# Optimization experiments

Measured on AMD Instinct MI355X. Metric: run time of the kernel, lower is better.

The kernel has to match this reference:

```python
import jax, jax.numpy as jnp
import numpy as np

K = 16

def _knn_idx(pts, k):
    # pts: [B, 3, N] -> idx [B, N, k] (self-inclusive nearest neighbors)
    inner = -2.0 * jnp.einsum('bdn,bdm->bnm', pts, pts)
    xx = jnp.sum(pts * pts, axis=1)  # [B, N]
    pd = -xx[:, :, None] - inner - xx[:, None, :]  # negative squared distance
    _, idx = jax.lax.top_k(pd, k)
    return idx

def _gather(feats, idx):
    # feats: [B, N, D], idx: [B, N, k] -> [B, N, k, D]
    return jax.vmap(lambda f, i: f[i])(feats, idx)

def _conv1x1(x, w, b):
    # x: [B, Cin, N], w: [Cout, Cin], b: [Cout]
    return jnp.einsum('oi,bin->bon', w, x) + b[None, :, None]

def _linear(x, w, b):
    # x: [B, N, Din], w: [Dout, Din]
    return jnp.einsum('bnd,od->bno', x, w) + b

def _local_cov(pts, idx):
    # pts: [B, 3, N] -> [B, 12, N]
    nb = _gather(jnp.swapaxes(pts, 1, 2), idx)  # [B, N, k, 3]
    outer = nb[:, :, 0, :, None] * nb[:, :, 1, None, :]  # [B, N, 3, 3]
    B, N = pts.shape[0], pts.shape[2]
    outer = jnp.swapaxes(outer.reshape(B, N, 9), 1, 2)  # [B, 9, N]
    return jnp.concatenate([pts, outer], axis=1)

def _local_maxpool(x, idx):
    # x: [B, D, N] -> [B, N, D]
    nb = _gather(jnp.swapaxes(x, 1, 2), idx)  # [B, N, k, D]
    return jnp.max(nb, axis=2)

def setup_inputs() -> dict:
    key = jax.random.key(0)
    ks = jax.random.split(key, 20)
    def w(k, shape):
        return jax.random.normal(k, shape, dtype=jnp.float32) * 0.05
    pts = jax.random.normal(ks[0], (8, 3, 4096), dtype=jnp.float32)
    return {
        'pts': pts,
        'm1w1': w(ks[1], (64, 12)), 'm1b1': w(ks[2], (64,)),
        'm1w2': w(ks[3], (64, 64)), 'm1b2': w(ks[4], (64,)),
        'm1w3': w(ks[5], (64, 64)), 'm1b3': w(ks[6], (64,)),
        'l1w': w(ks[7], (64, 64)), 'l1b': w(ks[8], (64,)),
        'c1w': w(ks[9], (128, 64)), 'c1b': w(ks[10], (128,)),
        'l2w': w(ks[11], (128, 128)), 'l2b': w(ks[12], (128,)),
        'c2w': w(ks[13], (1024, 128)), 'c2b': w(ks[14], (1024,)),
        'm2w1': w(ks[15], (512, 1024)), 'm2b1': w(ks[16], (512,)),
        'm2w2': w(ks[17], (512, 512)), 'm2b2': w(ks[18], (512,)),
    }

def reference(pts, m1w1, m1b1, m1w2, m1b2, m1w3, m1b3, l1w, l1b,
              c1w, c1b, l2w, l2b, c2w, c2b, m2w1, m2b1, m2w2, m2b2):
    idx = _knn_idx(pts, K)  # [B, N, k]
    x = _local_cov(pts, idx)  # [B, 12, N]
    # mlp1: three 1x1 convs with ReLU
    x = jax.nn.relu(_conv1x1(x, m1w1, m1b1))
    x = jax.nn.relu(_conv1x1(x, m1w2, m1b2))
    x = jax.nn.relu(_conv1x1(x, m1w3, m1b3))  # [B, 64, N]
    # graph layer
    x = _local_maxpool(x, idx)          # [B, N, 64]
    x = _linear(x, l1w, l1b)            # [B, N, 64]
    x = jnp.swapaxes(x, 1, 2)           # [B, 64, N]
    x = jax.nn.relu(_conv1x1(x, c1w, c1b))  # [B, 128, N]
    x = _local_maxpool(x, idx)          # [B, N, 128]
    x = _linear(x, l2w, l2b)            # [B, N, 128]
    x = jnp.swapaxes(x, 1, 2)           # [B, 128, N]
    x = _conv1x1(x, c2w, c2b)           # [B, 1024, N]
    # global max pool
    x = jnp.max(x, axis=2, keepdims=True)  # [B, 1024, 1]
    # mlp2
    x = jax.nn.relu(_conv1x1(x, m2w1, m2b1))
    x = _conv1x1(x, m2w2, m2b2)  # [B, 512, 1]
    return x.reshape(-1, 512)
```

## Files before the change

### kernel.cpp

```cpp
#include <hip/hip_runtime.h>
#include <cfloat>

#define NBATCH 8
#define NPTS   4096
#define KNN    16
#define PPB    32
#define NSL    8
#define CAP    24

typedef unsigned short u16;
typedef __attribute__((ext_vector_type(8))) short short8;
typedef __attribute__((ext_vector_type(4))) float f32x4;

__device__ __forceinline__ float relu_f(float x) { return x > 0.f ? x : 0.f; }

__device__ __forceinline__ void bf16_split(float v, u16& hi, u16& lo)
{
    unsigned u = __float_as_uint(v);
    unsigned hb = (u + 0x7FFFu + ((u >> 16) & 1u)) >> 16;
    float hf = __uint_as_float(hb << 16);
    float l = v - hf;
    unsigned ul = __float_as_uint(l);
    unsigned lb = (ul + 0x7FFFu + ((ul >> 16) & 1u)) >> 16;
    hi = (u16)hb; lo = (u16)lb;
}

__global__ __launch_bounds__(256)
void knn_kernel(const float* __restrict__ pts, int* __restrict__ idxout)
{
    __shared__ __align__(16) float4 tile[NSL * 129];
    __shared__ float  kl[PPB * NSL * 8];
    __shared__ float  thr[PPB];
    __shared__ int    cnt[PPB];

    const int b = blockIdx.y, tid = threadIdx.x;
    const int ptl = tid >> 3, r = tid & 7;
    const int n = blockIdx.x * PPB + ptl;
    const float* pb = pts + (size_t)b * 3 * NPTS;

    const float sx = pb[n], sy = pb[NPTS + n], sz = pb[2 * NPTS + n];

    float k8[8];
#pragma unroll
    for (int s = 0; s < 8; ++s) k8[s] = -FLT_MAX;

    const float4* slice = tile + r * 129;

    for (int t = 0; t < 4; ++t) {
        if (t) __syncthreads();
        for (int i = tid; i < 1024; i += 256) {
            int j = t * 1024 + i;
            float x = pb[j], y = pb[NPTS + j], z = pb[2 * NPTS + j];
            float xx = __fadd_rn(__fadd_rn(__fmul_rn(x, x), __fmul_rn(y, y)),
                                 __fmul_rn(z, z));
            tile[(i >> 7) * 129 + (i & 127)] = make_float4(x, y, z, xx);
        }
        __syncthreads();
#pragma unroll 8
        for (int ii = 0; ii < 128; ++ii) {
            float4 c = slice[ii];
            float dt = __fmaf_rn(sx, c.x, __fmaf_rn(sy, c.y, __fmul_rn(sz, c.z)));
            float pd = __fmaf_rn(2.f, dt, -c.w);
            float old0 = k8[0];
#pragma unroll
            for (int s = 7; s >= 1; --s)
                k8[s] = __builtin_amdgcn_fmed3f(k8[s - 1], k8[s], pd);
            k8[0] = fmaxf(old0, pd);
        }
    }

#pragma unroll
    for (int s = 0; s < 8; ++s) kl[(ptl * NSL + r) * 8 + s] = k8[s];
    __syncthreads();

    if (r == 0) {
        const float* L = kl + ptl * 64;
        int p0 = 0, p1 = 0, p2 = 0, p3 = 0, p4 = 0, p5 = 0, p6 = 0, p7 = 0;
        float tv = 0.f;
        for (int o = 0; o < 16; ++o) {
            float v0 = (p0 < 8) ? L[p0]      : -FLT_MAX;
            float v1 = (p1 < 8) ? L[8 + p1]  : -FLT_MAX;
            float v2 = (p2 < 8) ? L[16 + p2] : -FLT_MAX;
            float v3 = (p3 < 8) ? L[24 + p3] : -FLT_MAX;
            float v4 = (p4 < 8) ? L[32 + p4] : -FLT_MAX;
            float v5 = (p5 < 8) ? L[40 + p5] : -FLT_MAX;
            float v6 = (p6 < 8) ? L[48 + p6] : -FLT_MAX;
            float v7 = (p7 < 8) ? L[56 + p7] : -FLT_MAX;
            float m = fmaxf(fmaxf(fmaxf(v0, v1), fmaxf(v2, v3)),
                            fmaxf(fmaxf(v4, v5), fmaxf(v6, v7)));
            tv = m;
            if      (v0 == m) ++p0;
            else if (v1 == m) ++p1;
            else if (v2 == m) ++p2;
            else if (v3 == m) ++p3;
            else if (v4 == m) ++p4;
            else if (v5 == m) ++p5;
            else if (v6 == m) ++p6;
            else              ++p7;
        }
        thr[ptl] = tv;
        cnt[ptl] = 0;
    }
    __syncthreads();
    const float myThr = thr[ptl];

    float* pv = kl;
    int*   pi = (int*)(kl + PPB * CAP);

    for (int tt = 0; tt < 4; ++tt) {
        int t = 3 - tt;
        if (tt) {
            __syncthreads();
            for (int i = tid; i < 1024; i += 256) {
                int j = t * 1024 + i;
                float x = pb[j], y = pb[NPTS + j], z = pb[2 * NPTS + j];
                float xx = __fadd_rn(__fadd_rn(__fmul_rn(x, x), __fmul_rn(y, y)),
                                     __fmul_rn(z, z));
                tile[(i >> 7) * 129 + (i & 127)] = make_float4(x, y, z, xx);
            }
            __syncthreads();
        }
#pragma unroll 8
        for (int ii = 0; ii < 128; ++ii) {
            float4 c = slice[ii];
            float dt = __fmaf_rn(sx, c.x, __fmaf_rn(sy, c.y, __fmul_rn(sz, c.z)));
            float pd = __fmaf_rn(2.f, dt, -c.w);
            if (pd >= myThr) {
                int pos = atomicAdd(&cnt[ptl], 1);
                if (pos < CAP) {
                    pv[ptl * CAP + pos] = pd;
                    pi[ptl * CAP + pos] = t * 1024 + r * 128 + ii;
                }
            }
        }
    }
    __syncthreads();

    if (tid < PPB) {
        const int np = blockIdx.x * PPB + tid;
        int* out = idxout + ((size_t)b * NPTS + np) * KNN;
        int c = cnt[tid];
        if (c <= CAP) {
            float* v  = pv + tid * CAP;
            int*   ix = pi + tid * CAP;
            for (int o = 0; o < 16; ++o) {
                int best = o;
                for (int q = o + 1; q < c; ++q) {
                    float vq = v[q], vb = v[best];
                    if (vq > vb || (vq == vb && ix[q] < ix[best])) best = q;
                }
                float tv = v[o]; v[o] = v[best]; v[best] = tv;
                int   ti = ix[o]; ix[o] = ix[best]; ix[best] = ti;
                out[o] = ix[o];
            }
        } else {
            float qx = pb[np], qy = pb[NPTS + np], qz = pb[2 * NPTS + np];
            float v16[16]; int i16[16];
#pragma unroll
            for (int s = 0; s < 16; ++s) { v16[s] = -FLT_MAX; i16[s] = 0; }
            for (int j = 0; j < NPTS; ++j) {
                float x = pb[j], y = pb[NPTS + j], z = pb[2 * NPTS + j];
                float xx = __fadd_rn(__fadd_rn(__fmul_rn(x, x), __fmul_rn(y, y)),
                                     __fmul_rn(z, z));
                float dt = __fmaf_rn(qx, x, __fmaf_rn(qy, y, __fmul_rn(qz, z)));
                float pd = __fmaf_rn(2.f, dt, -xx);
                if (pd > v16[15]) {
                    int s = 15;
                    while (s > 0 && pd > v16[s - 1]) {
                        v16[s] = v16[s - 1]; i16[s] = i16[s - 1]; --s;
                    }
                    v16[s] = pd; i16[s] = j;
                }
            }
            for (int o = 0; o < 16; ++o) out[o] = i16[o];
        }
    }
}

__global__ __launch_bounds__(256)
void cov_mlp1_kernel(const float* __restrict__ pts, const int* __restrict__ idx,
                     const float* __restrict__ w1, const float* __restrict__ b1,
                     const float* __restrict__ w2, const float* __restrict__ b2,
                     const float* __restrict__ w3, const float* __restrict__ b3,
                     float* __restrict__ h3out)
{
    __shared__ __align__(16) float cov[64 * 16];
    __shared__ __align__(16) float w1s[64 * 16];
    __shared__ __align__(16) float w2s[64 * 68];
    __shared__ __align__(16) float w3s[64 * 68];
    __shared__ __align__(16) float hA[64 * 68];
    __shared__ __align__(16) float hB[64 * 68];

    const int b = blockIdx.y, tid = threadIdx.x;
    const int n0 = blockIdx.x * 64;
    const int pq = tid >> 4, cq = tid & 15;

    for (int i = tid; i < 64 * 4; i += 256) {
        int p = i >> 2, k4 = i & 3;
        float4 v = make_float4(0.f, 0.f, 0.f, 0.f);
        if (k4 < 3) v = *(const float4*)(w1 + p * 12 + k4 * 4);
        ((float4*)(w1s + p * 16))[k4] = v;
    }
    for (int i = tid; i < 64 * 16; i += 256) {
        int p = i >> 4, k4 = i & 15;
        ((float4*)(w2s + p * 68))[k4] = ((const float4*)(w2 + p * 64))[k4];
        ((float4*)(w3s + p * 68))[k4] = ((const float4*)(w3 + p * 64))[k4];
    }
    if (tid < 64) {
        const int n = n0 + tid;
        const int* ip = idx + ((size_t)b * NPTS + n) * KNN;
        int j0 = ip[0], j1 = ip[1];
        const float* pb = pts + (size_t)b * 3 * NPTS;
        float px = pb[n],  py = pb[NPTS + n],  pz = pb[2 * NPTS + n];
        float ax = pb[j0], ay = pb[NPTS + j0], az = pb[2 * NPTS + j0];
        float bx = pb[j1], by = pb[NPTS + j1], bz = pb[2 * NPTS + j1];
        float* cv = cov + tid * 16;
        cv[0] = px; cv[1] = py; cv[2] = pz;
        cv[3] = ax * bx; cv[4]  = ax * by; cv[5]  = ax * bz;
        cv[6] = ay * bx; cv[7]  = ay * by; cv[8]  = ay * bz;
        cv[9] = az * bx; cv[10] = az * by; cv[11] = az * bz;
        cv[12] = 0.f; cv[13] = 0.f; cv[14] = 0.f; cv[15] = 0.f;
    }
    __syncthreads();

    {
        float acc[4][4];
#pragma unroll
        for (int i = 0; i < 4; ++i)
#pragma unroll
            for (int j = 0; j < 4; ++j) acc[i][j] = 0.f;
        const float4* X4 = (const float4*)cov;
        const float4* W4 = (const float4*)w1s;
#pragma unroll
        for (int k4 = 0; k4 < 4; ++k4) {
            float4 xa[4], wb[4];
#pragma unroll
            for (int i = 0; i < 4; ++i) xa[i] = X4[(pq * 4 + i) * 4 + k4];
#pragma unroll
            for (int j = 0; j < 4; ++j) wb[j] = W4[(cq + 16 * j) * 4 + k4];
#pragma unroll
            for (int i = 0; i < 4; ++i)
#pragma unroll
                for (int j = 0; j < 4; ++j)
                    acc[i][j] += xa[i].x * wb[j].x + xa[i].y * wb[j].y
                               + xa[i].z * wb[j].z + xa[i].w * wb[j].w;
        }
#pragma unroll
        for (int j = 0; j < 4; ++j) {
            int c = cq + 16 * j;
            float bias = b1[c];
#pragma unroll
            for (int i = 0; i < 4; ++i)
                hA[(pq * 4 + i) * 68 + c] = relu_f(acc[i][j] + bias);
        }
    }
    __syncthreads();

    {
        float acc[4][4];
#pragma unroll
        for (int i = 0; i < 4; ++i)
#pragma unroll
            for (int j = 0; j < 4; ++j) acc[i][j] = 0.f;
        const float4* X4 = (const float4*)hA;
        const float4* W4 = (const float4*)w2s;
        for (int k4 = 0; k4 < 16; ++k4) {
            float4 xa[4], wb[4];
#pragma unroll
            for (int i = 0; i < 4; ++i) xa[i] = X4[(pq * 4 + i) * 17 + k4];
#pragma unroll
            for (int j = 0; j < 4; ++j) wb[j] = W4[(cq + 16 * j) * 17 + k4];
#pragma unroll
            for (int i = 0; i < 4; ++i)
#pragma unroll
                for (int j = 0; j < 4; ++j)
                    acc[i][j] += xa[i].x * wb[j].x + xa[i].y * wb[j].y
                               + xa[i].z * wb[j].z + xa[i].w * wb[j].w;
        }
#pragma unroll
        for (int j = 0; j < 4; ++j) {
            int c = cq + 16 * j;
            float bias = b2[c];
#pragma unroll
            for (int i = 0; i < 4; ++i)
                hB[(pq * 4 + i) * 68 + c] = relu_f(acc[i][j] + bias);
        }
    }
    __syncthreads();

    {
        float acc[4][4];
#pragma unroll
        for (int i = 0; i < 4; ++i)
#pragma unroll
            for (int j = 0; j < 4; ++j) acc[i][j] = 0.f;
        const float4* X4 = (const float4*)hB;
        const float4* W4 = (const float4*)w3s;
        for (int k4 = 0; k4 < 16; ++k4) {
            float4 xa[4], wb[4];
#pragma unroll
            for (int i = 0; i < 4; ++i) xa[i] = X4[(pq * 4 + i) * 17 + k4];
#pragma unroll
            for (int j = 0; j < 4; ++j) wb[j] = W4[(cq + 16 * j) * 17 + k4];
#pragma unroll
            for (int i = 0; i < 4; ++i)
#pragma unroll
                for (int j = 0; j < 4; ++j)
                    acc[i][j] += xa[i].x * wb[j].x + xa[i].y * wb[j].y
                               + xa[i].z * wb[j].z + xa[i].w * wb[j].w;
        }
#pragma unroll
        for (int j = 0; j < 4; ++j) {
            int c = cq + 16 * j;
            float bias = b3[c];
#pragma unroll
            for (int i = 0; i < 4; ++i)
                h3out[((size_t)b * NPTS + n0 + pq * 4 + i) * 64 + c] =
                    relu_f(acc[i][j] + bias);
        }
    }
}

template <int DV4>
__global__ __launch_bounds__(256)
void maxpool4_kernel(const float4* __restrict__ f, const int* __restrict__ idx,
                     float4* __restrict__ out)
{
    constexpr int SH = (DV4 == 16) ? 4 : 5;
    int t = blockIdx.x * 256 + threadIdx.x;
    int d4 = t & (DV4 - 1);
    int n  = (t >> SH) & (NPTS - 1);
    int b  = t >> (SH + 12);
    const int* ip = idx + ((size_t)b * NPTS + n) * KNN;
    const float4* fb = f + (size_t)b * NPTS * DV4;
    float4 v = make_float4(-FLT_MAX, -FLT_MAX, -FLT_MAX, -FLT_MAX);
#pragma unroll
    for (int k = 0; k < KNN; ++k) {
        float4 c = fb[(size_t)ip[k] * DV4 + d4];
        v.x = fmaxf(v.x, c.x); v.y = fmaxf(v.y, c.y);
        v.z = fmaxf(v.z, c.z); v.w = fmaxf(v.w, c.w);
    }
    out[t] = v;
}

__global__ __launch_bounds__(256)
void lin_conv1_kernel(const float* __restrict__ xin,
                      const float* __restrict__ l1w, const float* __restrict__ l1b,
                      const float* __restrict__ c1w, const float* __restrict__ c1b,
                      float* __restrict__ yout)
{
    __shared__ __align__(16) float sx[64 * 68];
    __shared__ __align__(16) float wbuf[64 * 68];
    __shared__ __align__(16) float t1[64 * 68];
    const int b = blockIdx.y, tid = threadIdx.x;
    const int n0 = blockIdx.x * 64;
    const int pq = tid >> 4, cq = tid & 15;

    for (int i = tid; i < 64 * 16; i += 256) {
        int p = i >> 4, k4 = i & 15;
        ((float4*)(sx + p * 68))[k4] =
            ((const float4*)(xin + ((size_t)b * NPTS + n0 + p) * 64))[k4];
        ((float4*)(wbuf + p * 68))[k4] = ((const float4*)(l1w + p * 64))[k4];
    }
    __syncthreads();

    {
        float acc[4][4];
#pragma unroll
        for (int i = 0; i < 4; ++i)
#pragma unroll
            for (int j = 0; j < 4; ++j) acc[i][j] = 0.f;
        const float4* X4 = (const float4*)sx;
        const float4* W4 = (const float4*)wbuf;
        for (int k4 = 0; k4 < 16; ++k4) {
            float4 xa[4], wb[4];
#pragma unroll
            for (int i = 0; i < 4; ++i) xa[i] = X4[(pq * 4 + i) * 17 + k4];
#pragma unroll
            for (int j = 0; j < 4; ++j) wb[j] = W4[(cq + 16 * j) * 17 + k4];
#pragma unroll
            for (int i = 0; i < 4; ++i)
#pragma unroll
                for (int j = 0; j < 4; ++j)
                    acc[i][j] += xa[i].x * wb[j].x + xa[i].y * wb[j].y
                               + xa[i].z * wb[j].z + xa[i].w * wb[j].w;
        }
#pragma unroll
        for (int j = 0; j < 4; ++j) {
            int c = cq + 16 * j;
            float bias = l1b[c];
#pragma unroll
            for (int i = 0; i < 4; ++i)
                t1[(pq * 4 + i) * 68 + c] = acc[i][j] + bias;
        }
    }

    for (int g = 0; g < 2; ++g) {
        __syncthreads();
        for (int i = tid; i < 64 * 16; i += 256) {
            int p = i >> 4, k4 = i & 15;
            ((float4*)(wbuf + p * 68))[k4] =
                ((const float4*)(c1w + (size_t)(g * 64 + p) * 64))[k4];
        }
        __syncthreads();
        float acc[4][4];
#pragma unroll
        for (int i = 0; i < 4; ++i)
#pragma unroll
            for (int j = 0; j < 4; ++j) acc[i][j] = 0.f;
        const float4* X4 = (const float4*)t1;
        const float4* W4 = (const float4*)wbuf;
        for (int k4 = 0; k4 < 16; ++k4) {
            float4 xa[4], wb[4];
#pragma unroll
            for (int i = 0; i < 4; ++i) xa[i] = X4[(pq * 4 + i) * 17 + k4];
#pragma unroll
            for (int j = 0; j < 4; ++j) wb[j] = W4[(cq + 16 * j) * 17 + k4];
#pragma unroll
            for (int i = 0; i < 4; ++i)
#pragma unroll
                for (int j = 0; j < 4; ++j)
                    acc[i][j] += xa[i].x * wb[j].x + xa[i].y * wb[j].y
                               + xa[i].z * wb[j].z + xa[i].w * wb[j].w;
        }
#pragma unroll
        for (int j = 0; j < 4; ++j) {
            int c = g * 64 + cq + 16 * j;
            float bias = c1b[c];
#pragma unroll
            for (int i = 0; i < 4; ++i)
                yout[((size_t)b * NPTS + n0 + pq * 4 + i) * 128 + c] =
                    relu_f(acc[i][j] + bias);
        }
    }
}

__global__ __launch_bounds__(256)
void lin2_kernel(const float* __restrict__ xin, const float* __restrict__ w,
                 const float* __restrict__ bias,
                 u16* __restrict__ xhi, u16* __restrict__ xlo)
{
    __shared__ __align__(16) float Xs[64 * 132];
    __shared__ __align__(16) float Ws[64 * 132];
    const int chunk = blockIdx.x, g = blockIdx.y, b = blockIdx.z;
    const int tid = threadIdx.x;

    for (int i = tid; i < 64 * 32; i += 256) {
        int p = i >> 5, k4 = i & 31;
        ((float4*)(Xs + p * 132))[k4] =
            ((const float4*)(xin + ((size_t)b * NPTS + chunk * 64 + p) * 128))[k4];
        ((float4*)(Ws + p * 132))[k4] =
            ((const float4*)(w + (size_t)(g * 64 + p) * 128))[k4];
    }
    __syncthreads();

    const int pq = tid >> 4, cq = tid & 15;
    const float4* X4 = (const float4*)Xs;
    const float4* W4 = (const float4*)Ws;
    float acc[4][4];
#pragma unroll
    for (int i = 0; i < 4; ++i)
#pragma unroll
        for (int j = 0; j < 4; ++j) acc[i][j] = 0.f;

    for (int k4 = 0; k4 < 32; ++k4) {
        float4 xa[4], wb[4];
#pragma unroll
        for (int i = 0; i < 4; ++i) xa[i] = X4[(pq * 4 + i) * 33 + k4];
#pragma unroll
        for (int j = 0; j < 4; ++j) wb[j] = W4[(cq + 16 * j) * 33 + k4];
#pragma unroll
        for (int i = 0; i < 4; ++i)
#pragma unroll
            for (int j = 0; j < 4; ++j)
                acc[i][j] += xa[i].x * wb[j].x + xa[i].y * wb[j].y
                           + xa[i].z * wb[j].z + xa[i].w * wb[j].w;
    }
#pragma unroll
    for (int j = 0; j < 4; ++j) {
        int c = g * 64 + cq + 16 * j;
        float bv = bias[c];
#pragma unroll
        for (int i = 0; i < 4; ++i) {
            float v = acc[i][j] + bv;
            size_t oidx = ((size_t)b * NPTS + chunk * 64 + pq * 4 + i) * 128 + c;
            u16 h, l;
            bf16_split(v, h, l);
            xhi[oidx] = h; xlo[oidx] = l;
        }
    }
}

__global__ __launch_bounds__(256)
void wsplit_kernel(const float* __restrict__ w, u16* __restrict__ whi,
                   u16* __restrict__ wlo)
{
    int t = blockIdx.x * 256 + threadIdx.x;
    u16 h, l;
    bf16_split(w[t], h, l);
    whi[t] = h; wlo[t] = l;
}

__global__ __launch_bounds__(256)
void conv2max_mfma(const u16* __restrict__ xhi, const u16* __restrict__ xlo,
                   const u16* __restrict__ whi, const u16* __restrict__ wlo,
                   const float* __restrict__ bias, float* __restrict__ pmax)
{
    __shared__ __align__(16) u16 lds[4 * 16384];
    u16* Wh = lds;
    u16* Wl = lds + 16384;
    u16* Xh = lds + 2 * 16384;
    u16* Xl = lds + 3 * 16384;

    const int chunk = blockIdx.x, g = blockIdx.y, b = blockIdx.z;
    const int tid = threadIdx.x;
    const int lane = tid & 63, wave = tid >> 6;
    const int l15 = lane & 15, l4 = lane >> 4;
    const int wm = wave >> 1, wn = wave & 1;

    const u16* wh_g = whi + (size_t)g * 128 * 128;
    const u16* wl_g = wlo + (size_t)g * 128 * 128;
    const u16* xh_g = xhi + ((size_t)b * NPTS + chunk * 128) * 128;
    const u16* xl_g = xlo + ((size_t)b * NPTS + chunk * 128) * 128;

    for (int u = tid; u < 2048; u += 256) {
        int row = u & 127, seg = u >> 7;
        int lo_ = seg * 1024 + row * 8;
        int go_ = row * 128 + seg * 8;
        *(short8*)&Wh[lo_] = *(const short8*)&wh_g[go_];
        *(short8*)&Wl[lo_] = *(const short8*)&wl_g[go_];
        *(short8*)&Xh[lo_] = *(const short8*)&xh_g[go_];
        *(short8*)&Xl[lo_] = *(const short8*)&xl_g[go_];
    }
    __syncthreads();

    f32x4 acc[4][4];
#pragma unroll
    for (int mt = 0; mt < 4; ++mt)
#pragma unroll
        for (int nt = 0; nt < 4; ++nt)
            acc[mt][nt] = (f32x4){0.f, 0.f, 0.f, 0.f};

    for (int kb = 0; kb < 4; ++kb) {
        const int seg = kb * 4 + l4;
        short8 Ah[4], Al[4], Bh[4], Bl[4];
#pragma unroll
        for (int mt = 0; mt < 4; ++mt) {
            int off = seg * 1024 + (wm * 64 + mt * 16 + l15) * 8;
            Ah[mt] = *(const short8*)&Wh[off];
            Al[mt] = *(const short8*)&Wl[off];
        }
#pragma unroll
        for (int nt = 0; nt < 4; ++nt) {
            int off = seg * 1024 + (wn * 64 + nt * 16 + l15) * 8;
            Bh[nt] = *(const short8*)&Xh[off];
            Bl[nt] = *(const short8*)&Xl[off];
        }
#pragma unroll
        for (int mt = 0; mt < 4; ++mt)
#pragma unroll
            for (int nt = 0; nt < 4; ++nt) {
                acc[mt][nt] = __builtin_amdgcn_mfma_f32_16x16x32_bf16(
                    Ah[mt], Bh[nt], acc[mt][nt], 0, 0, 0);
                acc[mt][nt] = __builtin_amdgcn_mfma_f32_16x16x32_bf16(
                    Ah[mt], Bl[nt], acc[mt][nt], 0, 0, 0);
                acc[mt][nt] = __builtin_amdgcn_mfma_f32_16x16x32_bf16(
                    Al[mt], Bh[nt], acc[mt][nt], 0, 0, 0);
            }
    }

    __syncthreads();
    float* smax = (float*)lds;
#pragma unroll
    for (int mt = 0; mt < 4; ++mt)
#pragma unroll
        for (int r = 0; r < 4; ++r) {
            float m = fmaxf(fmaxf(acc[mt][0][r], acc[mt][1][r]),
                            fmaxf(acc[mt][2][r], acc[mt][3][r]));
            int c = wm * 64 + mt * 16 + 4 * l4 + r;
            smax[c * 33 + wn * 16 + l15] = m;
        }
    __syncthreads();
    if (tid < 128) {
        const float* row = smax + tid * 33;
        float v = row[0];
#pragma unroll
        for (int j = 1; j < 32; ++j) v = fmaxf(v, row[j]);
        int c = g * 128 + tid;
        pmax[((size_t)b * 32 + chunk) * 1024 + c] = v + bias[c];
    }
}

__global__ __launch_bounds__(256)
void gmax_kernel(const float* __restrict__ pmax, float* __restrict__ gmax)
{
    int t = blockIdx.x * 256 + threadIdx.x;
    int b = t >> 10, ch = t & 1023;
    const float* pp = pmax + (size_t)b * 32 * 1024 + ch;
    float v = -FLT_MAX;
    for (int c = 0; c < 32; ++c) v = fmaxf(v, pp[c * 1024]);
    gmax[t] = v;
}

__global__ __launch_bounds__(128)
void mlp2a_kernel(const float* __restrict__ g, const float* __restrict__ w1,
                  const float* __restrict__ b1, float* __restrict__ h)
{
    __shared__ __align__(16) float sg[1024];
    const int b = blockIdx.y, tid = threadIdx.x;
    for (int i = tid; i < 1024; i += 128) sg[i] = g[b * 1024 + i];
    __syncthreads();
    const int ch = blockIdx.x * 128 + tid;
    const float4* xr = (const float4*)sg;
    const float4* wr = (const float4*)(w1 + (size_t)ch * 1024);
    float a0 = 0.f, a1 = 0.f, a2 = 0.f, a3 = 0.f;
    for (int k = 0; k < 256; ++k) {
        float4 w = wr[k], x = xr[k];
        a0 += w.x * x.x; a1 += w.y * x.y; a2 += w.z * x.z; a3 += w.w * x.w;
    }
    h[b * 512 + ch] = relu_f(b1[ch] + ((a0 + a1) + (a2 + a3)));
}

__global__ __launch_bounds__(128)
void mlp2b_kernel(const float* __restrict__ h, const float* __restrict__ w2,
                  const float* __restrict__ b2, float* __restrict__ out)
{
    __shared__ __align__(16) float sh[512];
    const int b = blockIdx.y, tid = threadIdx.x;
    for (int i = tid; i < 512; i += 128) sh[i] = h[b * 512 + i];
    __syncthreads();
    const int ch = blockIdx.x * 128 + tid;
    const float4* xr = (const float4*)sh;
    const float4* wr = (const float4*)(w2 + (size_t)ch * 512);
    float a0 = 0.f, a1 = 0.f, a2 = 0.f, a3 = 0.f;
    for (int k = 0; k < 128; ++k) {
        float4 w = wr[k], x = xr[k];
        a0 += w.x * x.x; a1 += w.y * x.y; a2 += w.z * x.z; a3 += w.w * x.w;
    }
    out[b * 512 + ch] = b2[ch] + ((a0 + a1) + (a2 + a3));
}

extern "C" void kernel_launch(void* const* d_in, const int* in_sizes, int n_in,
                              void* d_out, int out_size, void* d_ws, size_t ws_size,
                              hipStream_t stream)
{
    const float* pts  = (const float*)d_in[0];
    const float* m1w1 = (const float*)d_in[1];
    const float* m1b1 = (const float*)d_in[2];
    const float* m1w2 = (const float*)d_in[3];
    const float* m1b2 = (const float*)d_in[4];
    const float* m1w3 = (const float*)d_in[5];
    const float* m1b3 = (const float*)d_in[6];
    const float* l1w  = (const float*)d_in[7];
    const float* l1b  = (const float*)d_in[8];
    const float* c1w  = (const float*)d_in[9];
    const float* c1b  = (const float*)d_in[10];
    const float* l2w  = (const float*)d_in[11];
    const float* l2b  = (const float*)d_in[12];
    const float* c2w  = (const float*)d_in[13];
    const float* c2b  = (const float*)d_in[14];
    const float* m2w1 = (const float*)d_in[15];
    const float* m2b1 = (const float*)d_in[16];
    const float* m2w2 = (const float*)d_in[17];
    const float* m2b2 = (const float*)d_in[18];

    char* ws = (char*)d_ws;
    size_t off = 0;
    int*   idx   = (int*)(ws + off);   off += (size_t)NBATCH * NPTS * KNN * 4;
    float* h3    = (float*)(ws + off); off += (size_t)NBATCH * NPTS * 64 * 4;
    float* mp1   = (float*)(ws + off); off += (size_t)NBATCH * NPTS * 64 * 4;
    float* y1    = (float*)(ws + off); off += (size_t)NBATCH * NPTS * 128 * 4;
    float* mp2   = (float*)(ws + off); off += (size_t)NBATCH * NPTS * 128 * 4;
    float* pmaxb = (float*)(ws + off); off += (size_t)NBATCH * 64 * 1024 * 4;
    float* gmx   = (float*)(ws + off); off += (size_t)NBATCH * 1024 * 4;
    float* hbuf  = (float*)(ws + off); off += (size_t)NBATCH * 512 * 4;
    u16*   whi   = (u16*)(ws + off);   off += (size_t)1024 * 128 * 2;
    u16*   wlo   = (u16*)(ws + off);   off += (size_t)1024 * 128 * 2;
    u16*   xhi   = (u16*)y1;
    u16*   xlo   = (u16*)((char*)y1 + (size_t)NBATCH * NPTS * 128 * 2);

    wsplit_kernel<<<dim3(512), 256, 0, stream>>>(c2w, whi, wlo);
    knn_kernel<<<dim3(NPTS / PPB, NBATCH), 256, 0, stream>>>(pts, idx);
    cov_mlp1_kernel<<<dim3(64, NBATCH), 256, 0, stream>>>(pts, idx, m1w1, m1b1,
                                                          m1w2, m1b2, m1w3, m1b3, h3);
    maxpool4_kernel<16><<<dim3(NBATCH * NPTS * 16 / 256), 256, 0, stream>>>(
        (const float4*)h3, idx, (float4*)mp1);
    lin_conv1_kernel<<<dim3(64, NBATCH), 256, 0, stream>>>(mp1, l1w, l1b, c1w, c1b, y1);
    maxpool4_kernel<32><<<dim3(NBATCH * NPTS * 32 / 256), 256, 0, stream>>>(
        (const float4*)y1, idx, (float4*)mp2);
    lin2_kernel<<<dim3(64, 2, NBATCH), 256, 0, stream>>>(mp2, l2w, l2b, xhi, xlo);
    conv2max_mfma<<<dim3(32, 8, NBATCH), 256, 0, stream>>>(xhi, xlo, whi, wlo,
                                                           c2b, pmaxb);
    gmax_kernel<<<dim3(32), 256, 0, stream>>>(pmaxb, gmx);
    mlp2a_kernel<<<dim3(4, NBATCH), 128, 0, stream>>>(gmx, m2w1, m2b1, hbuf);
    mlp2b_kernel<<<dim3(4, NBATCH), 128, 0, stream>>>(hbuf, m2w2, m2b2, (float*)d_out);
}
```

Baseline: 319.1 us.

## Halve KNN points per block with 16 slices; pack bf16 hi/lo into u32

The KNN kernel now handles 16 points per block with 16 threads each, so every thread scans 64 candidates instead of 128. That doubles the grid size and shortens the serial top-8 insertion chain, at the cost of a 16-way merge per point. Separately, the bf16 hi/lo split of activations and conv2 weights is stored as one packed u32 array instead of two u16 arrays. conv2max unpacks it with perm instructions, which makes each global store a single 4-byte write, at the cost of extra ALU work during the LDS fill.

```diff
diff --git a/kernel.cpp b/kernel.cpp
--- a/kernel.cpp
+++ b/kernel.cpp
@@ -4,17 +4,18 @@
 #define NBATCH 8
 #define NPTS   4096
 #define KNN    16
-#define PPB    32
-#define NSL    8
+#define PPB    16
+#define NSL    16
 #define CAP    24
 
 typedef unsigned short u16;
+typedef unsigned int   u32;
 typedef __attribute__((ext_vector_type(8))) short short8;
 typedef __attribute__((ext_vector_type(4))) float f32x4;
 
 __device__ __forceinline__ float relu_f(float x) { return x > 0.f ? x : 0.f; }
 
-__device__ __forceinline__ void bf16_split(float v, u16& hi, u16& lo)
+__device__ __forceinline__ u32 bf16_split_pack(float v)
 {
     unsigned u = __float_as_uint(v);
     unsigned hb = (u + 0x7FFFu + ((u >> 16) & 1u)) >> 16;
@@ -22,19 +23,33 @@
     float l = v - hf;
     unsigned ul = __float_as_uint(l);
     unsigned lb = (ul + 0x7FFFu + ((ul >> 16) & 1u)) >> 16;
-    hi = (u16)hb; lo = (u16)lb;
+    return (hb << 16) | (lb & 0xFFFFu);
+}
+
+__device__ __forceinline__ void unpack8(uint4 a, uint4 b, short8& h, short8& l)
+{
+    union { unsigned u[4]; short8 s; } H, L;
+    H.u[0] = __builtin_amdgcn_perm(a.y, a.x, 0x07060302);
+    H.u[1] = __builtin_amdgcn_perm(a.w, a.z, 0x07060302);
+    H.u[2] = __builtin_amdgcn_perm(b.y, b.x, 0x07060302);
+    H.u[3] = __builtin_amdgcn_perm(b.w, b.z, 0x07060302);
+    L.u[0] = __builtin_amdgcn_perm(a.y, a.x, 0x05040100);
+    L.u[1] = __builtin_amdgcn_perm(a.w, a.z, 0x05040100);
+    L.u[2] = __builtin_amdgcn_perm(b.y, b.x, 0x05040100);
+    L.u[3] = __builtin_amdgcn_perm(b.w, b.z, 0x05040100);
+    h = H.s; l = L.s;
 }
 
 __global__ __launch_bounds__(256)
 void knn_kernel(const float* __restrict__ pts, int* __restrict__ idxout)
 {
-    __shared__ __align__(16) float4 tile[NSL * 129];
+    __shared__ __align__(16) float4 tile[8 * 129];
     __shared__ float  kl[PPB * NSL * 8];
     __shared__ float  thr[PPB];
     __shared__ int    cnt[PPB];
 
     const int b = blockIdx.y, tid = threadIdx.x;
-    const int ptl = tid >> 3, r = tid & 7;
+    const int ptl = tid >> 4, r = tid & 15;
     const int n = blockIdx.x * PPB + ptl;
     const float* pb = pts + (size_t)b * 3 * NPTS;
 
@@ -44,7 +59,7 @@
 #pragma unroll
     for (int s = 0; s < 8; ++s) k8[s] = -FLT_MAX;
 
-    const float4* slice = tile + r * 129;
+    const float4* slice = tile + (r >> 1) * 129 + (r & 1) * 64;
 
     for (int t = 0; t < 4; ++t) {
         if (t) __syncthreads();
@@ -57,7 +72,7 @@
         }
         __syncthreads();
 #pragma unroll 8
-        for (int ii = 0; ii < 128; ++ii) {
+        for (int ii = 0; ii < 64; ++ii) {
             float4 c = slice[ii];
             float dt = __fmaf_rn(sx, c.x, __fmaf_rn(sy, c.y, __fmul_rn(sz, c.z)));
             float pd = __fmaf_rn(2.f, dt, -c.w);
@@ -74,29 +89,21 @@
     __syncthreads();
 
     if (r == 0) {
-        const float* L = kl + ptl * 64;
-        int p0 = 0, p1 = 0, p2 = 0, p3 = 0, p4 = 0, p5 = 0, p6 = 0, p7 = 0;
+        const float* L = kl + ptl * (NSL * 8);
+        int p[NSL];
+#pragma unroll
+        for (int l = 0; l < NSL; ++l) p[l] = 0;
         float tv = 0.f;
         for (int o = 0; o < 16; ++o) {
-            float v0 = (p0 < 8) ? L[p0]      : -FLT_MAX;
-            float v1 = (p1 < 8) ? L[8 + p1]  : -FLT_MAX;
-            float v2 = (p2 < 8) ? L[16 + p2] : -FLT_MAX;
-            float v3 = (p3 < 8) ? L[24 + p3] : -FLT_MAX;
-            float v4 = (p4 < 8) ? L[32 + p4] : -FLT_MAX;
-            float v5 = (p5 < 8) ? L[40 + p5] : -FLT_MAX;
-            float v6 = (p6 < 8) ? L[48 + p6] : -FLT_MAX;
-            float v7 = (p7 < 8) ? L[56 + p7] : -FLT_MAX;
-            float m = fmaxf(fmaxf(fmaxf(v0, v1), fmaxf(v2, v3)),
-                            fmaxf(fmaxf(v4, v5), fmaxf(v6, v7)));
-            tv = m;
-            if      (v0 == m) ++p0;
-            else if (v1 == m) ++p1;
-            else if (v2 == m) ++p2;
-            else if (v3 == m) ++p3;
-            else if (v4 == m) ++p4;
-            else if (v5 == m) ++p5;
-            else if (v6 == m) ++p6;
-            else              ++p7;
+            float best = -FLT_MAX; int bi = 0;
+#pragma unroll
+            for (int l = 0; l < NSL; ++l) {
+                float v = (p[l] < 8) ? L[l * 8 + p[l]] : -FLT_MAX;
+                if (v > best) { best = v; bi = l; }
+            }
+#pragma unroll
+            for (int l = 0; l < NSL; ++l) p[l] += (l == bi);
+            tv = best;
         }
         thr[ptl] = tv;
         cnt[ptl] = 0;
@@ -121,7 +128,7 @@
             __syncthreads();
         }
 #pragma unroll 8
-        for (int ii = 0; ii < 128; ++ii) {
+        for (int ii = 0; ii < 64; ++ii) {
             float4 c = slice[ii];
             float dt = __fmaf_rn(sx, c.x, __fmaf_rn(sy, c.y, __fmul_rn(sz, c.z)));
             float pd = __fmaf_rn(2.f, dt, -c.w);
@@ -129,7 +136,7 @@
                 int pos = atomicAdd(&cnt[ptl], 1);
                 if (pos < CAP) {
                     pv[ptl * CAP + pos] = pd;
-                    pi[ptl * CAP + pos] = t * 1024 + r * 128 + ii;
+                    pi[ptl * CAP + pos] = t * 1024 + r * 64 + ii;
                 }
             }
         }
@@ -437,8 +444,7 @@
 
 __global__ __launch_bounds__(256)
 void lin2_kernel(const float* __restrict__ xin, const float* __restrict__ w,
-                 const float* __restrict__ bias,
-                 u16* __restrict__ xhi, u16* __restrict__ xlo)
+                 const float* __restrict__ bias, u32* __restrict__ xpk)
 {
     __shared__ __align__(16) float Xs[64 * 132];
     __shared__ __align__(16) float Ws[64 * 132];
@@ -484,26 +490,20 @@
         for (int i = 0; i < 4; ++i) {
             float v = acc[i][j] + bv;
             size_t oidx = ((size_t)b * NPTS + chunk * 64 + pq * 4 + i) * 128 + c;
-            u16 h, l;
-            bf16_split(v, h, l);
-            xhi[oidx] = h; xlo[oidx] = l;
-        }
-    }
-}
-
-__global__ __launch_bounds__(256)
-void wsplit_kernel(const float* __restrict__ w, u16* __restrict__ whi,
-                   u16* __restrict__ wlo)
+            xpk[oidx] = bf16_split_pack(v);
+        }
+    }
+}
+
+__global__ __launch_bounds__(256)
+void wsplit_kernel(const float* __restrict__ w, u32* __restrict__ wpk)
 {
     int t = blockIdx.x * 256 + threadIdx.x;
-    u16 h, l;
-    bf16_split(w[t], h, l);
-    whi[t] = h; wlo[t] = l;
-}
-
-__global__ __launch_bounds__(256)
-void conv2max_mfma(const u16* __restrict__ xhi, const u16* __restrict__ xlo,
-                   const u16* __restrict__ whi, const u16* __restrict__ wlo,
+    wpk[t] = bf16_split_pack(w[t]);
+}
+
+__global__ __launch_bounds__(256)
+void conv2max_mfma(const u32* __restrict__ xpk, const u32* __restrict__ wpk,
                    const float* __restrict__ bias, float* __restrict__ pmax)
 {
     __shared__ __align__(16) u16 lds[4 * 16384];
@@ -518,19 +518,22 @@
     const int l15 = lane & 15, l4 = lane >> 4;
     const int wm = wave >> 1, wn = wave & 1;
 
-    const u16* wh_g = whi + (size_t)g * 128 * 128;
-    const u16* wl_g = wlo + (size_t)g * 128 * 128;
-    const u16* xh_g = xhi + ((size_t)b * NPTS + chunk * 128) * 128;
-    const u16* xl_g = xlo + ((size_t)b * NPTS + chunk * 128) * 128;
+    const u32* wp_g = wpk + (size_t)g * 128 * 128;
+    const u32* xp_g = xpk + ((size_t)b * NPTS + chunk * 128) * 128;
 
     for (int u = tid; u < 2048; u += 256) {
         int row = u & 127, seg = u >> 7;
+        int go = row * 128 + seg * 8;
         int lo_ = seg * 1024 + row * 8;
-        int go_ = row * 128 + seg * 8;
-        *(short8*)&Wh[lo_] = *(const short8*)&wh_g[go_];
-        *(short8*)&Wl[lo_] = *(const short8*)&wl_g[go_];
-        *(short8*)&Xh[lo_] = *(const short8*)&xh_g[go_];
-        *(short8*)&Xl[lo_] = *(const short8*)&xl_g[go_];
+        uint4 a = *(const uint4*)&wp_g[go];
+        uint4 b4 = *(const uint4*)&wp_g[go + 4];
+        short8 h, l;
+        unpack8(a, b4, h, l);
+        *(short8*)&Wh[lo_] = h; *(short8*)&Wl[lo_] = l;
+        a = *(const uint4*)&xp_g[go];
+        b4 = *(const uint4*)&xp_g[go + 4];
+        unpack8(a, b4, h, l);
+        *(short8*)&Xh[lo_] = h; *(short8*)&Xl[lo_] = l;
     }
     __syncthreads();
 
@@ -674,12 +677,10 @@
     float* pmaxb = (float*)(ws + off); off += (size_t)NBATCH * 64 * 1024 * 4;
     float* gmx   = (float*)(ws + off); off += (size_t)NBATCH * 1024 * 4;
     float* hbuf  = (float*)(ws + off); off += (size_t)NBATCH * 512 * 4;
-    u16*   whi   = (u16*)(ws + off);   off += (size_t)1024 * 128 * 2;
-    u16*   wlo   = (u16*)(ws + off);   off += (size_t)1024 * 128 * 2;
-    u16*   xhi   = (u16*)y1;
-    u16*   xlo   = (u16*)((char*)y1 + (size_t)NBATCH * NPTS * 128 * 2);
-
-    wsplit_kernel<<<dim3(512), 256, 0, stream>>>(c2w, whi, wlo);
+    u32*   wpk   = (u32*)(ws + off);   off += (size_t)1024 * 128 * 4;
+    u32*   xpk   = (u32*)y1;
+
+    wsplit_kernel<<<dim3(512), 256, 0, stream>>>(c2w, wpk);
     knn_kernel<<<dim3(NPTS / PPB, NBATCH), 256, 0, stream>>>(pts, idx);
     cov_mlp1_kernel<<<dim3(64, NBATCH), 256, 0, stream>>>(pts, idx, m1w1, m1b1,
                                                           m1w2, m1b2, m1w3, m1b3, h3);
@@ -688,9 +689,8 @@
     lin_conv1_kernel<<<dim3(64, NBATCH), 256, 0, stream>>>(mp1, l1w, l1b, c1w, c1b, y1);
     maxpool4_kernel<32><<<dim3(NBATCH * NPTS * 32 / 256), 256, 0, stream>>>(
         (const float4*)y1, idx, (float4*)mp2);
-    lin2_kernel<<<dim3(64, 2, NBATCH), 256, 0, stream>>>(mp2, l2w, l2b, xhi, xlo);
-    conv2max_mfma<<<dim3(32, 8, NBATCH), 256, 0, stream>>>(xhi, xlo, whi, wlo,
-                                                           c2b, pmaxb);
+    lin2_kernel<<<dim3(64, 2, NBATCH), 256, 0, stream>>>(mp2, l2w, l2b, xpk);
+    conv2max_mfma<<<dim3(32, 8, NBATCH), 256, 0, stream>>>(xpk, wpk, c2b, pmaxb);
     gmax_kernel<<<dim3(32), 256, 0, stream>>>(pmaxb, gmx);
     mlp2a_kernel<<<dim3(4, NBATCH), 128, 0, stream>>>(gmx, m2w1, m2b1, hbuf);
     mlp2b_kernel<<<dim3(4, NBATCH), 128, 0, stream>>>(hbuf, m2w2, m2b2, (float*)d_out);
```

Measured after the change: 333.3 us. 4.4% more time.
